# Performance work log

Measured on AMD Instinct MI355X. Metric: run time of the kernel, lower is better.

The kernel has to match this reference:

```python
import jax, jax.numpy as jnp
import numpy as np

S = 8    # number of path-segments
U = 32   # per-segment input width (subscript 'u')
V = 32   # per-segment output width (subscript 'v')
C = 32   # number of weight groups (indexed dimension)
Z = 65536  # number of rows


def setup_inputs() -> dict:
    key = jax.random.key(0)
    k1, k2, k3 = jax.random.split(key, 3)
    input1 = jax.random.normal(k1, (C, S * U * V), dtype=jnp.float32) * 0.05  # grouped weights
    input2 = jax.random.normal(k2, (Z, S * U), dtype=jnp.float32)             # row features
    counts = jnp.full((C,), Z // C, dtype=jnp.int32)                          # rows per group, contiguous
    coefficients = jax.random.uniform(k3, (S,), dtype=jnp.float32, minval=0.5, maxval=1.5)
    return {"input1": input1, "input2": input2, "counts": counts, "coefficients": coefficients}


def reference(input1, input2, counts, coefficients):
    # Segment-indexed grouped linear: rows are contiguous per group (sizes = counts).
    # For each path-segment s: out_s[z, v] = coeff_s * sum_u x_s[z, u] * W_s[g(z), u, v]
    # Final output concatenates the S segment outputs along the last dim.
    seg_ids = jnp.repeat(jnp.arange(C, dtype=jnp.int32), counts, total_repeat_length=Z)  # [Z]
    outs = []
    for s in range(S):
        W = input1[:, s * U * V:(s + 1) * U * V].reshape(C, U, V)  # [C,U,V]
        x = input2[:, s * U:(s + 1) * U]                           # [Z,U]
        Wz = W[seg_ids]                                            # [Z,U,V] gather by group
        outs.append(coefficients[s] * jnp.einsum('zu,zuv->zv', x, Wz))
    return jnp.concatenate(outs, axis=-1)  # [Z, S*V]
```

## Files before the change

### kernel.cpp

```cpp
#include <hip/hip_runtime.h>


constexpr int S = 8, U = 32, V = 32, C = 32, Z = 65536;
constexpr int SU = S * U;
constexpr int SV = S * V;
constexpr int NT = 256;
constexpr int BZ = 32;
constexpr int TPB = 4;

typedef float    f4     __attribute__((ext_vector_type(4)));
typedef float    f32x16 __attribute__((ext_vector_type(16)));
typedef short    bf16x8 __attribute__((ext_vector_type(8)));
typedef unsigned u32x4  __attribute__((ext_vector_type(4)));

typedef const __attribute__((address_space(1))) unsigned gu32;
typedef __attribute__((address_space(3))) unsigned lu32;

__device__ __forceinline__ short f2bf(float f) {
  unsigned u = __builtin_bit_cast(unsigned, f);
  u = (u + 0x7FFFu + ((u >> 16) & 1u)) >> 16;
  return (short)u;
}

__device__ __forceinline__ unsigned cvtpk(float lo, float hi) {
  unsigned r;
  asm("v_cvt_pk_bf16_f32 %0, %1, %2" : "=v"(r) : "v"(lo), "v"(hi));
  return r;
}

__device__ __forceinline__ int xidx(int m, int c) {
  return ((m >> 3) << 9) + ((c >> 3) << 6) + ((c & 7) << 3) + (m & 7);
}

__global__ __launch_bounds__(NT) void IndexedLinear_kernel(
    const float* __restrict__ W_all,
    const float* __restrict__ X,
    const int*   __restrict__ counts,
    const float* __restrict__ coeff,
    float*       __restrict__ out)
{
  const int tid  = threadIdx.x;
  const int lane = tid & 63;
  const int w    = tid >> 6;
  const int zb   = blockIdx.x * (BZ * TPB);

  __shared__ f4 XL[2][BZ * 64];

  int cnt = (lane < C) ? counts[lane] : 0;
  int inc = cnt;
  #pragma unroll
  for (int d = 1; d < 32; d <<= 1) {
    int o = __shfl_up(inc, d, 64);
    if (lane >= d) inc += o;
  }
  const int exc = inc - cnt;

  const int m  = lane & 31;
  const int h  = lane >> 5;
  const int s0 = 2 * w;

  {
    const char* gb = (const char*)X
        + (size_t)(zb + 8 * w + (lane & 7)) * (SU * 4) + (lane >> 3) * 16;
    #pragma unroll
    for (int k = 0; k < 8; ++k)
      __builtin_amdgcn_global_load_lds((gu32*)(gb + k * 128),
                                       (lu32*)&XL[0][(8 * w + k) * 64], 16, 0, 0);
  }

  int curseg = -1;
  bf16x8 b1[2], b2[2];

  for (int t = 0; t < TPB; ++t) {
    const int z0   = zb + t * BZ;
    const int bsel = t & 1;

    const unsigned long long ma = __ballot(lane < C && exc <= z0);
    const unsigned long long mb = __ballot(lane < C && exc <= z0 + BZ - 1);
    const int segA = __popcll(ma) - 1;
    const int segB = __popcll(mb) - 1;
    const bool uni = (segA == segB);

    if (uni && segA != curseg) {
      curseg = segA;
      const float* wseg = W_all + (size_t)segA * (S * U * V);
      #pragma unroll
      for (int tt = 0; tt < 2; ++tt) {
        const int s = s0 + tt;
        const float cs = coeff[s];
        const float* wb = wseg + s * (U * V);
        #pragma unroll
        for (int j = 0; j < 8; ++j)
          b1[tt][j] = f2bf(wb[(8 * h + j) * V + m] * cs);
        #pragma unroll
        for (int j = 0; j < 8; ++j)
          b2[tt][j] = f2bf(wb[(16 + 8 * h + j) * V + m] * cs);
      }
    }

    if (t + 1 < TPB) {
      const char* gb = (const char*)X
          + (size_t)(z0 + BZ + 8 * w + (lane & 7)) * (SU * 4) + (lane >> 3) * 16;
      #pragma unroll
      for (int k = 0; k < 8; ++k)
        __builtin_amdgcn_global_load_lds((gu32*)(gb + k * 128),
                                         (lu32*)&XL[bsel ^ 1][(8 * w + k) * 64],
                                         16, 0, 0);
      asm volatile("s_waitcnt vmcnt(8)" ::: "memory");
    } else {
      asm volatile("s_waitcnt vmcnt(0)" ::: "memory");
    }
    __builtin_amdgcn_s_barrier();
    asm volatile("" ::: "memory");

    if (uni) {
      #pragma unroll
      for (int tt = 0; tt < 2; ++tt) {
        const int s = s0 + tt;
        const f4 xa = XL[bsel][xidx(m, s * 8 + 2 * h)];
        const f4 xb = XL[bsel][xidx(m, s * 8 + 2 * h + 1)];
        const f4 xc = XL[bsel][xidx(m, s * 8 + 4 + 2 * h)];
        const f4 xd = XL[bsel][xidx(m, s * 8 + 4 + 2 * h + 1)];
        u32x4 pa, pb;
        pa[0] = cvtpk(xa[0], xa[1]); pa[1] = cvtpk(xa[2], xa[3]);
        pa[2] = cvtpk(xb[0], xb[1]); pa[3] = cvtpk(xb[2], xb[3]);
        pb[0] = cvtpk(xc[0], xc[1]); pb[1] = cvtpk(xc[2], xc[3]);
        pb[2] = cvtpk(xd[0], xd[1]); pb[3] = cvtpk(xd[2], xd[3]);
        const bf16x8 a1 = __builtin_bit_cast(bf16x8, pa);
        const bf16x8 a2 = __builtin_bit_cast(bf16x8, pb);
        f32x16 acc = {};
        acc = __builtin_amdgcn_mfma_f32_32x32x16_bf16(a1, b1[tt], acc, 0, 0, 0);
        acc = __builtin_amdgcn_mfma_f32_32x32x16_bf16(a2, b2[tt], acc, 0, 0, 0);

        float* ob = out + (size_t)z0 * SV + s * V + m;
        #pragma unroll
        for (int r = 0; r < 16; ++r) {
          const int row = (r & 3) + 8 * (r >> 2) + 4 * h;
          __builtin_nontemporal_store(acc[r], ob + (size_t)row * SV);
        }
      }
    } else {
      const int zz = z0 + m;
      int sg = 0;
      #pragma unroll 1
      for (int i = 1; i < C; ++i) {
        const int pi = __shfl(exc, i, 64);
        if (pi <= zz) sg = i;
      }
      #pragma unroll 1
      for (int tt = 0; tt < 2; ++tt) {
        const int s = s0 + tt;
        const float cs = coeff[s];
        const float* wr = W_all + (size_t)sg * (S * U * V) + s * (U * V) + 16 * h;
        float accv[16] = {};
        #pragma unroll 1
        for (int cq = 0; cq < 8; ++cq) {
          const f4 xv = XL[bsel][xidx(m, s * 8 + cq)];
          #pragma unroll
          for (int ii = 0; ii < 4; ++ii) {
            const int u = cq * 4 + ii;
            const float xu = xv[ii];
            #pragma unroll
            for (int j = 0; j < 16; ++j) accv[j] += xu * wr[u * V + j];
          }
        }
        float* ob = out + (size_t)zz * SV + s * V + 16 * h;
        #pragma unroll
        for (int j = 0; j < 16; ++j) ob[j] = accv[j] * cs;
      }
    }

    asm volatile("" ::: "memory");
    __builtin_amdgcn_s_barrier();
  }
}

extern "C" void kernel_launch(void* const* d_in, const int* in_sizes, int n_in,
                              void* d_out, int out_size, void* d_ws, size_t ws_size,
                              hipStream_t stream) {
  const float* input1       = (const float*)d_in[0];
  const float* input2       = (const float*)d_in[1];
  const int*   counts       = (const int*)d_in[2];
  const float* coefficients = (const float*)d_in[3];
  float*       out          = (float*)d_out;

  const int grid = Z / (BZ * TPB);
  IndexedLinear_kernel<<<grid, NT, 0, stream>>>(input1, input2, counts,
                                                coefficients, out);
}
```

Baseline: 118.2 us.

## Drop LDS double-buffering; load X directly to registers, one tile per block

Removes the shared-memory double-buffered async X staging and the multi-tile loop per block. Each block now handles a single 32-row tile, loading X straight from global memory into registers, and the grid grows four-fold. Weight conversion now uses the packed bf16 convert instruction. The aim is to drop the barriers and LDS round trip and to gain parallelism from more blocks. In exchange, the weight fragments are reloaded once per tile instead of being reused across tiles, and the direct per-lane X loads are less coalesced.

```diff
diff --git a/kernel.cpp b/kernel.cpp
--- a/kernel.cpp
+++ b/kernel.cpp
@@ -6,30 +6,16 @@
 constexpr int SV = S * V;
 constexpr int NT = 256;
 constexpr int BZ = 32;
-constexpr int TPB = 4;
 
 typedef float    f4     __attribute__((ext_vector_type(4)));
 typedef float    f32x16 __attribute__((ext_vector_type(16)));
 typedef short    bf16x8 __attribute__((ext_vector_type(8)));
 typedef unsigned u32x4  __attribute__((ext_vector_type(4)));
 
-typedef const __attribute__((address_space(1))) unsigned gu32;
-typedef __attribute__((address_space(3))) unsigned lu32;
-
-__device__ __forceinline__ short f2bf(float f) {
-  unsigned u = __builtin_bit_cast(unsigned, f);
-  u = (u + 0x7FFFu + ((u >> 16) & 1u)) >> 16;
-  return (short)u;
-}
-
 __device__ __forceinline__ unsigned cvtpk(float lo, float hi) {
   unsigned r;
   asm("v_cvt_pk_bf16_f32 %0, %1, %2" : "=v"(r) : "v"(lo), "v"(hi));
   return r;
-}
-
-__device__ __forceinline__ int xidx(int m, int c) {
-  return ((m >> 3) << 9) + ((c >> 3) << 6) + ((c & 7) << 3) + (m & 7);
 }
 
 __global__ __launch_bounds__(NT) void IndexedLinear_kernel(
@@ -42,9 +28,11 @@
   const int tid  = threadIdx.x;
   const int lane = tid & 63;
   const int w    = tid >> 6;
-  const int zb   = blockIdx.x * (BZ * TPB);
+  const int z0   = blockIdx.x * BZ;
 
-  __shared__ f4 XL[2][BZ * 64];
+  const int m  = lane & 31;
+  const int h  = lane >> 5;
+  const int s0 = 2 * w;
 
   int cnt = (lane < C) ? counts[lane] : 0;
   int inc = cnt;
@@ -54,124 +42,94 @@
     if (lane >= d) inc += o;
   }
   const int exc = inc - cnt;
+  const unsigned long long ma = __ballot(lane < C && exc <= z0);
+  const unsigned long long mb = __ballot(lane < C && exc <= z0 + BZ - 1);
+  const int segA = __popcll(ma) - 1;
+  const int segB = __popcll(mb) - 1;
+  const bool uni = (segA == segB);
 
-  const int m  = lane & 31;
-  const int h  = lane >> 5;
-  const int s0 = 2 * w;
+  if (uni) {
+    const f4* Xr = (const f4*)X + (size_t)(z0 + m) * (SU / 4) + 2 * h;
+    f4 xs[8];
+    #pragma unroll
+    for (int tt = 0; tt < 2; ++tt) {
+      const int c0 = (s0 + tt) * 8;
+      xs[4 * tt + 0] = Xr[c0 + 0];
+      xs[4 * tt + 1] = Xr[c0 + 1];
+      xs[4 * tt + 2] = Xr[c0 + 4];
+      xs[4 * tt + 3] = Xr[c0 + 5];
+    }
 
-  {
-    const char* gb = (const char*)X
-        + (size_t)(zb + 8 * w + (lane & 7)) * (SU * 4) + (lane >> 3) * 16;
+    const float* wseg = W_all + (size_t)segA * (S * U * V);
+    u32x4 b1[2], b2[2];
     #pragma unroll
-    for (int k = 0; k < 8; ++k)
-      __builtin_amdgcn_global_load_lds((gu32*)(gb + k * 128),
-                                       (lu32*)&XL[0][(8 * w + k) * 64], 16, 0, 0);
-  }
-
-  int curseg = -1;
-  bf16x8 b1[2], b2[2];
-
-  for (int t = 0; t < TPB; ++t) {
-    const int z0   = zb + t * BZ;
-    const int bsel = t & 1;
-
-    const unsigned long long ma = __ballot(lane < C && exc <= z0);
-    const unsigned long long mb = __ballot(lane < C && exc <= z0 + BZ - 1);
-    const int segA = __popcll(ma) - 1;
-    const int segB = __popcll(mb) - 1;
-    const bool uni = (segA == segB);
-
-    if (uni && segA != curseg) {
-      curseg = segA;
-      const float* wseg = W_all + (size_t)segA * (S * U * V);
+    for (int tt = 0; tt < 2; ++tt) {
+      const int s = s0 + tt;
+      const float cs = coeff[s];
+      const float* wb = wseg + s * (U * V) + m;
       #pragma unroll
-      for (int tt = 0; tt < 2; ++tt) {
-        const int s = s0 + tt;
-        const float cs = coeff[s];
-        const float* wb = wseg + s * (U * V);
-        #pragma unroll
-        for (int j = 0; j < 8; ++j)
-          b1[tt][j] = f2bf(wb[(8 * h + j) * V + m] * cs);
-        #pragma unroll
-        for (int j = 0; j < 8; ++j)
-          b2[tt][j] = f2bf(wb[(16 + 8 * h + j) * V + m] * cs);
+      for (int j = 0; j < 4; ++j) {
+        b1[tt][j] = cvtpk(wb[(8 * h + 2 * j) * V] * cs,
+                          wb[(8 * h + 2 * j + 1) * V] * cs);
+        b2[tt][j] = cvtpk(wb[(16 + 8 * h + 2 * j) * V] * cs,
+                          wb[(16 + 8 * h + 2 * j + 1) * V] * cs);
       }
     }
 
-    if (t + 1 < TPB) {
-      const char* gb = (const char*)X
-          + (size_t)(z0 + BZ + 8 * w + (lane & 7)) * (SU * 4) + (lane >> 3) * 16;
+    #pragma unroll
+    for (int tt = 0; tt < 2; ++tt) {
+      const int s = s0 + tt;
+      const f4 xa = xs[4 * tt + 0], xb = xs[4 * tt + 1];
+      const f4 xc = xs[4 * tt + 2], xd = xs[4 * tt + 3];
+      u32x4 pa, pb;
+      pa[0] = cvtpk(xa[0], xa[1]); pa[1] = cvtpk(xa[2], xa[3]);
+      pa[2] = cvtpk(xb[0], xb[1]); pa[3] = cvtpk(xb[2], xb[3]);
+      pb[0] = cvtpk(xc[0], xc[1]); pb[1] = cvtpk(xc[2], xc[3]);
+      pb[2] = cvtpk(xd[0], xd[1]); pb[3] = cvtpk(xd[2], xd[3]);
+      const bf16x8 a1 = __builtin_bit_cast(bf16x8, pa);
+      const bf16x8 a2 = __builtin_bit_cast(bf16x8, pb);
+      f32x16 acc = {};
+      acc = __builtin_amdgcn_mfma_f32_32x32x16_bf16(
+          a1, __builtin_bit_cast(bf16x8, b1[tt]), acc, 0, 0, 0);
+      acc = __builtin_amdgcn_mfma_f32_32x32x16_bf16(
+          a2, __builtin_bit_cast(bf16x8, b2[tt]), acc, 0, 0, 0);
+
+      float* ob = out + (size_t)z0 * SV + s * V + m;
       #pragma unroll
-      for (int k = 0; k < 8; ++k)
-        __builtin_amdgcn_global_load_lds((gu32*)(gb + k * 128),
-                                         (lu32*)&XL[bsel ^ 1][(8 * w + k) * 64],
-                                         16, 0, 0);
-      asm volatile("s_waitcnt vmcnt(8)" ::: "memory");
-    } else {
-      asm volatile("s_waitcnt vmcnt(0)" ::: "memory");
+      for (int r = 0; r < 16; ++r) {
+        const int row = (r & 3) + 8 * (r >> 2) + 4 * h;
+        __builtin_nontemporal_store(acc[r], ob + (size_t)row * SV);
+      }
     }
-    __builtin_amdgcn_s_barrier();
-    asm volatile("" ::: "memory");
-
-    if (uni) {
-      #pragma unroll
-      for (int tt = 0; tt < 2; ++tt) {
-        const int s = s0 + tt;
-        const f4 xa = XL[bsel][xidx(m, s * 8 + 2 * h)];
-        const f4 xb = XL[bsel][xidx(m, s * 8 + 2 * h + 1)];
-        const f4 xc = XL[bsel][xidx(m, s * 8 + 4 + 2 * h)];
-        const f4 xd = XL[bsel][xidx(m, s * 8 + 4 + 2 * h + 1)];
-        u32x4 pa, pb;
-        pa[0] = cvtpk(xa[0], xa[1]); pa[1] = cvtpk(xa[2], xa[3]);
-        pa[2] = cvtpk(xb[0], xb[1]); pa[3] = cvtpk(xb[2], xb[3]);
-        pb[0] = cvtpk(xc[0], xc[1]); pb[1] = cvtpk(xc[2], xc[3]);
-        pb[2] = cvtpk(xd[0], xd[1]); pb[3] = cvtpk(xd[2], xd[3]);
-        const bf16x8 a1 = __builtin_bit_cast(bf16x8, pa);
-        const bf16x8 a2 = __builtin_bit_cast(bf16x8, pb);
-        f32x16 acc = {};
-        acc = __builtin_amdgcn_mfma_f32_32x32x16_bf16(a1, b1[tt], acc, 0, 0, 0);
-        acc = __builtin_amdgcn_mfma_f32_32x32x16_bf16(a2, b2[tt], acc, 0, 0, 0);
-
-        float* ob = out + (size_t)z0 * SV + s * V + m;
+  } else {
+    const int zz = z0 + m;
+    int sg = 0;
+    #pragma unroll 1
+    for (int i = 1; i < C; ++i) {
+      const int pi = __shfl(exc, i, 64);
+      if (pi <= zz) sg = i;
+    }
+    #pragma unroll 1
+    for (int tt = 0; tt < 2; ++tt) {
+      const int s = s0 + tt;
+      const float cs = coeff[s];
+      const float* wr = W_all + (size_t)sg * (S * U * V) + s * (U * V) + 16 * h;
+      float accv[16] = {};
+      #pragma unroll 1
+      for (int cq = 0; cq < 8; ++cq) {
+        const f4 xv = ((const f4*)X)[(size_t)zz * (SU / 4) + s * 8 + cq];
         #pragma unroll
-        for (int r = 0; r < 16; ++r) {
-          const int row = (r & 3) + 8 * (r >> 2) + 4 * h;
-          __builtin_nontemporal_store(acc[r], ob + (size_t)row * SV);
+        for (int ii = 0; ii < 4; ++ii) {
+          const int u = cq * 4 + ii;
+          const float xu = xv[ii];
+          #pragma unroll
+          for (int j = 0; j < 16; ++j) accv[j] += xu * wr[u * V + j];
         }
       }
-    } else {
-      const int zz = z0 + m;
-      int sg = 0;
-      #pragma unroll 1
-      for (int i = 1; i < C; ++i) {
-        const int pi = __shfl(exc, i, 64);
-        if (pi <= zz) sg = i;
-      }
-      #pragma unroll 1
-      for (int tt = 0; tt < 2; ++tt) {
-        const int s = s0 + tt;
-        const float cs = coeff[s];
-        const float* wr = W_all + (size_t)sg * (S * U * V) + s * (U * V) + 16 * h;
-        float accv[16] = {};
-        #pragma unroll 1
-        for (int cq = 0; cq < 8; ++cq) {
-          const f4 xv = XL[bsel][xidx(m, s * 8 + cq)];
-          #pragma unroll
-          for (int ii = 0; ii < 4; ++ii) {
-            const int u = cq * 4 + ii;
-            const float xu = xv[ii];
-            #pragma unroll
-            for (int j = 0; j < 16; ++j) accv[j] += xu * wr[u * V + j];
-          }
-        }
-        float* ob = out + (size_t)zz * SV + s * V + 16 * h;
-        #pragma unroll
-        for (int j = 0; j < 16; ++j) ob[j] = accv[j] * cs;
-      }
+      float* ob = out + (size_t)zz * SV + s * V + 16 * h;
+      #pragma unroll
+      for (int j = 0; j < 16; ++j) ob[j] = accv[j] * cs;
     }
-
-    asm volatile("" ::: "memory");
-    __builtin_amdgcn_s_barrier();
   }
 }
 
@@ -184,7 +142,7 @@
   const float* coefficients = (const float*)d_in[3];
   float*       out          = (float*)d_out;
 
-  const int grid = Z / (BZ * TPB);
+  const int grid = Z / BZ;
   IndexedLinear_kernel<<<grid, NT, 0, stream>>>(input1, input2, counts,
                                                 coefficients, out);
 }
```

New measurement: 120.7 us. +2.2%, slower.
